# Optimization experiments

Measured on AMD Instinct MI355X. Metric: run time of the kernel, lower is better.

## Reference

```python
import jax, jax.numpy as jnp
import numpy as np

N = 50000          # nodes
E = 800000         # directed edges (before self-loops)
IN_C = 512
HID = 256
HEADS = 8
HEAD_C = HID // HEADS
OUT_C = 64
NEG_SLOPE = 0.2    # PyG GATConv default LeakyReLU slope
EPS = 1e-16        # PyG softmax denominator epsilon


def _gat_layer(h, src, dst, a_src, a_dst):
    """One GATConv propagate step (eval mode, no attention dropout).
    h: [N, H, C] transformed node features; src/dst: [Etot] edge endpoints.
    Returns aggregated [N, H, C]."""
    # per-node attention logits: [N, H]
    alpha_src = jnp.einsum('nhc,hc->nh', h, a_src)
    alpha_dst = jnp.einsum('nhc,hc->nh', h, a_dst)
    e = alpha_src[src] + alpha_dst[dst]                      # [Etot, H]
    e = jnp.where(e > 0, e, NEG_SLOPE * e)                   # LeakyReLU
    # segment softmax over incoming edges of each dst node
    e_max = jax.ops.segment_max(e, dst, num_segments=N)      # [N, H]
    e_exp = jnp.exp(e - e_max[dst])                          # [Etot, H]
    denom = jax.ops.segment_sum(e_exp, dst, num_segments=N)  # [N, H]
    alpha = e_exp / (denom[dst] + EPS)                       # [Etot, H]
    msg = alpha[:, :, None] * h[src]                         # [Etot, H, C]
    return jax.ops.segment_sum(msg, dst, num_segments=N)     # [N, H, C]


def setup_inputs() -> dict:
    key = jax.random.key(0)
    ks = jax.random.split(key, 10)
    s1 = 1.0 / np.sqrt(IN_C)
    s2 = 1.0 / np.sqrt(HID)
    return {
        'x': jax.random.normal(ks[0], (N, IN_C), jnp.float32),
        'edge_index': jax.random.randint(ks[1], (2, E), 0, N, dtype=jnp.int64),
        'W1': jax.random.normal(ks[2], (IN_C, HID), jnp.float32) * s1,
        'a_src1': jax.random.normal(ks[3], (HEADS, HEAD_C), jnp.float32) * 0.1,
        'a_dst1': jax.random.normal(ks[4], (HEADS, HEAD_C), jnp.float32) * 0.1,
        'b1': jnp.zeros((HID,), jnp.float32),
        'W2': jax.random.normal(ks[5], (HID, OUT_C), jnp.float32) * s2,
        'a_src2': jax.random.normal(ks[6], (1, OUT_C), jnp.float32) * 0.1,
        'a_dst2': jax.random.normal(ks[7], (1, OUT_C), jnp.float32) * 0.1,
        'b2': jnp.zeros((OUT_C,), jnp.float32),
    }


def reference(x, edge_index, W1, a_src1, a_dst1, b1, W2, a_src2, a_dst2, b2):
    # PyG GATConv: add self-loops (default add_self_loops=True)
    loops = jnp.arange(N, dtype=edge_index.dtype)
    src = jnp.concatenate([edge_index[0], loops])
    dst = jnp.concatenate([edge_index[1], loops])

    # conv1: heads=8, concat=True
    h1 = (x @ W1).reshape(N, HEADS, HEAD_C)
    h1 = _gat_layer(h1, src, dst, a_src1, a_dst1).reshape(N, HID) + b1
    h1 = jax.nn.elu(h1)

    # conv2: heads=1, concat=False (mean over 1 head == identity)
    h2 = (h1 @ W2).reshape(N, 1, OUT_C)
    out = _gat_layer(h2, src, dst, a_src2, a_dst2).mean(axis=1) + b2
    return out
```

## Files before the change

kernel.cpp:

```cpp
#include <hip/hip_runtime.h>

#define N_NODES 50000
#define M_PAD   50048
#define NBLK    196
#define E_EDGES 800000
#define E_TOT   (E_EDGES + N_NODES)
#define IN_C 512
#define HID 256
#define HEADS 8
#define OUT_C 64

typedef unsigned int uint;
typedef unsigned short ushort_t;
typedef __bf16 bf16x8 __attribute__((ext_vector_type(8)));
typedef float f32x4 __attribute__((ext_vector_type(4)));
typedef float f32x2 __attribute__((ext_vector_type(2)));

__device__ __forceinline__ float lrelu(float x) { return x > 0.f ? x : 0.2f * x; }

__device__ __forceinline__ unsigned short f2bf(float f) {
  uint u = __float_as_uint(f);
  u += 0x7FFF + ((u >> 16) & 1);
  return (unsigned short)(u >> 16);
}
__device__ __forceinline__ float bflo(uint u) { return __uint_as_float(u << 16); }
__device__ __forceinline__ float bfhi(uint u) { return __uint_as_float(u & 0xFFFF0000u); }
__device__ __forceinline__ f32x2 unp2(uint u) {
  f32x2 r; r.x = bflo(u); r.y = bfhi(u); return r;
}

__global__ void k_count(const int* __restrict__ ei, int* __restrict__ counts) {
  int e = blockIdx.x * blockDim.x + threadIdx.x;
  if (e >= E_TOT) return;
  int d = (e < E_EDGES) ? ei[E_EDGES + e] : (e - E_EDGES);
  atomicAdd(&counts[d], 1);
}

__global__ void k_bsum(const int* __restrict__ counts, int* __restrict__ bsum) {
  int i = blockIdx.x * 256 + threadIdx.x;
  int v = (i < N_NODES) ? counts[i] : 0;
  __shared__ int ws[4];
  int lane = threadIdx.x & 63, wid = threadIdx.x >> 6;
  #pragma unroll
  for (int off = 32; off; off >>= 1) v += __shfl_xor(v, off);
  if (lane == 0) ws[wid] = v;
  __syncthreads();
  if (threadIdx.x == 0) bsum[blockIdx.x] = ws[0] + ws[1] + ws[2] + ws[3];
}

__global__ void k_bscan(const int* __restrict__ bsum, int* __restrict__ boff) {
  int tid = threadIdx.x;
  int v = (tid < NBLK) ? bsum[tid] : 0;
  int lane = tid & 63, wid = tid >> 6;
  int x = v;
  #pragma unroll
  for (int off = 1; off < 64; off <<= 1) {
    int t = __shfl_up(x, off);
    if (lane >= off) x += t;
  }
  __shared__ int ws[4];
  if (lane == 63) ws[wid] = x;
  __syncthreads();
  int woff = 0;
  for (int w = 0; w < wid; w++) woff += ws[w];
  if (tid < NBLK) boff[tid] = x + woff - v;
}

__global__ void k_local(const int* __restrict__ counts, const int* __restrict__ boff,
                        int* __restrict__ indptr, int* __restrict__ wptr) {
  int b = blockIdx.x;
  int i = b * 256 + threadIdx.x;
  int v = (i < N_NODES) ? counts[i] : 0;
  int lane = threadIdx.x & 63, wid = threadIdx.x >> 6;
  int x = v;
  #pragma unroll
  for (int off = 1; off < 64; off <<= 1) {
    int t = __shfl_up(x, off);
    if (lane >= off) x += t;
  }
  __shared__ int ws[4];
  if (lane == 63) ws[wid] = x;
  __syncthreads();
  int woff = boff[b];
  for (int w = 0; w < wid; w++) woff += ws[w];
  int excl = woff + x - v;
  if (i < N_NODES) { indptr[i] = excl; wptr[i] = excl; }
  if (b == 0 && threadIdx.x == 0) indptr[N_NODES] = E_TOT;
}

__global__ void k_scatter(const int* __restrict__ ei, int* __restrict__ wptr,
                          int* __restrict__ csr_src) {
  int e = blockIdx.x * blockDim.x + threadIdx.x;
  if (e >= E_TOT) return;
  int s, d;
  if (e < E_EDGES) { s = ei[e]; d = ei[E_EDGES + e]; }
  else { s = d = e - E_EDGES; }
  int pos = atomicAdd(&wptr[d], 1);
  csr_src[pos] = s;
}

__global__ void k_conv_w1(const float* __restrict__ W1, ushort_t* __restrict__ w1t) {
  int t = blockIdx.x * blockDim.x + threadIdx.x;
  if (t >= HID * IN_C) return;
  int n = t >> 9, k = t & 511;
  w1t[t] = f2bf(W1[(size_t)k * HID + n]);
}
__global__ void k_conv_w2(const float* __restrict__ W2, ushort_t* __restrict__ w2t) {
  int t = blockIdx.x * blockDim.x + threadIdx.x;
  if (t >= OUT_C * HID) return;
  int n = t >> 8, k = t & 255;
  w2t[t] = f2bf(W2[(size_t)k * OUT_C + n]);
}

__global__ __launch_bounds__(512) void k_mm1(const float* __restrict__ A,
                                             const ushort_t* __restrict__ Bt,
                                             ushort_t* __restrict__ Cb) {
  __shared__ ushort_t sA[128][40];
  __shared__ ushort_t sB[256][40];
  int tid = threadIdx.x;
  int wid = tid >> 6, lane = tid & 63;
  int wm = wid >> 2, wn = wid & 3;
  int lr = lane & 15, kg = lane >> 4;
  int row0 = blockIdx.x * 128;
  f32x4 acc[4][4] = {};

  for (int k0 = 0; k0 < IN_C; k0 += 32) {
    {
      int r = tid >> 2, cs = (tid & 3) * 8;
      int gr = row0 + r;
      unsigned short v[8];
      if (gr < N_NODES) {
        const float* src = A + (size_t)gr * IN_C + k0 + cs;
        float4 f0 = *reinterpret_cast<const float4*>(src);
        float4 f1 = *reinterpret_cast<const float4*>(src + 4);
        v[0] = f2bf(f0.x); v[1] = f2bf(f0.y); v[2] = f2bf(f0.z); v[3] = f2bf(f0.w);
        v[4] = f2bf(f1.x); v[5] = f2bf(f1.y); v[6] = f2bf(f1.z); v[7] = f2bf(f1.w);
      } else {
        #pragma unroll
        for (int i = 0; i < 8; i++) v[i] = 0;
      }
      uint4 pk;
      pk.x = v[0] | ((uint)v[1] << 16); pk.y = v[2] | ((uint)v[3] << 16);
      pk.z = v[4] | ((uint)v[5] << 16); pk.w = v[6] | ((uint)v[7] << 16);
      *reinterpret_cast<uint4*>(&sA[r][cs]) = pk;
    }
    {
      int n = tid >> 1, ks = (tid & 1) * 16;
      const ushort_t* src = Bt + (size_t)n * IN_C + k0 + ks;
      uint4 v0 = *reinterpret_cast<const uint4*>(src);
      uint4 v1 = *reinterpret_cast<const uint4*>(src + 8);
      *reinterpret_cast<uint4*>(&sB[n][ks]) = v0;
      *reinterpret_cast<uint4*>(&sB[n][ks + 8]) = v1;
    }
    __syncthreads();

    bf16x8 af[4], bfr[4];
    #pragma unroll
    for (int i = 0; i < 4; i++)
      af[i] = *reinterpret_cast<const bf16x8*>(&sA[wm * 64 + i * 16 + lr][kg * 8]);
    #pragma unroll
    for (int j = 0; j < 4; j++)
      bfr[j] = *reinterpret_cast<const bf16x8*>(&sB[wn * 64 + j * 16 + lr][kg * 8]);
    #pragma unroll
    for (int i = 0; i < 4; i++)
      #pragma unroll
      for (int j = 0; j < 4; j++)
        acc[i][j] = __builtin_amdgcn_mfma_f32_16x16x32_bf16(af[i], bfr[j], acc[i][j], 0, 0, 0);
    __syncthreads();
  }

  #pragma unroll
  for (int i = 0; i < 4; i++) {
    #pragma unroll
    for (int j = 0; j < 4; j++) {
      int gc = wn * 64 + j * 16 + lr;
      #pragma unroll
      for (int q = 0; q < 4; q++) {
        int gr = row0 + wm * 64 + i * 16 + kg * 4 + q;
        if (gr < N_NODES) Cb[(size_t)gr * HID + gc] = f2bf(acc[i][j][q]);
      }
    }
  }
}

__global__ __launch_bounds__(256) void k_mm2(const ushort_t* __restrict__ At,
                                             const ushort_t* __restrict__ Bt,
                                             float* __restrict__ C) {
  __shared__ ushort_t sA[128][40];
  __shared__ ushort_t sB[64][40];
  int tid = threadIdx.x;
  int wid = tid >> 6, lane = tid & 63;
  int lr = lane & 15, kg = lane >> 4;
  int row0 = blockIdx.x * 128;
  f32x4 acc[2][4] = {};

  for (int kt = 0; kt < HID / 32; ++kt) {
    {
      const ushort_t* src = At + ((size_t)blockIdx.x * 8 + kt) * 4096 + tid * 16;
      uint4 v0 = *reinterpret_cast<const uint4*>(src);
      uint4 v1 = *reinterpret_cast<const uint4*>(src + 8);
      int r = tid >> 1, ks = (tid & 1) * 16;
      *reinterpret_cast<uint4*>(&sA[r][ks]) = v0;
      *reinterpret_cast<uint4*>(&sA[r][ks + 8]) = v1;
    }
    if (tid < 128) {
      int n = tid >> 1, ks = (tid & 1) * 16;
      const ushort_t* src = Bt + (size_t)n * HID + kt * 32 + ks;
      uint4 v0 = *reinterpret_cast<const uint4*>(src);
      uint4 v1 = *reinterpret_cast<const uint4*>(src + 8);
      *reinterpret_cast<uint4*>(&sB[n][ks]) = v0;
      *reinterpret_cast<uint4*>(&sB[n][ks + 8]) = v1;
    }
    __syncthreads();

    bf16x8 af[2], bfr[4];
    #pragma unroll
    for (int i = 0; i < 2; i++)
      af[i] = *reinterpret_cast<const bf16x8*>(&sA[wid * 32 + i * 16 + lr][kg * 8]);
    #pragma unroll
    for (int j = 0; j < 4; j++)
      bfr[j] = *reinterpret_cast<const bf16x8*>(&sB[j * 16 + lr][kg * 8]);
    #pragma unroll
    for (int i = 0; i < 2; i++)
      #pragma unroll
      for (int j = 0; j < 4; j++)
        acc[i][j] = __builtin_amdgcn_mfma_f32_16x16x32_bf16(af[i], bfr[j], acc[i][j], 0, 0, 0);
    __syncthreads();
  }

  #pragma unroll
  for (int i = 0; i < 2; i++) {
    #pragma unroll
    for (int j = 0; j < 4; j++) {
      int gc = j * 16 + lr;
      #pragma unroll
      for (int q = 0; q < 4; q++) {
        int gr = row0 + wid * 32 + i * 16 + kg * 4 + q;
        if (gr < N_NODES) C[(size_t)gr * OUT_C + gc] = acc[i][j][q];
      }
    }
  }
}

__global__ void k_alpha1(const ushort_t* __restrict__ h1b, const float* __restrict__ a_src,
                         const float* __restrict__ a_dst, float* __restrict__ as1,
                         float* __restrict__ ad1) {
  int t = blockIdx.x * blockDim.x + threadIdx.x;
  if (t >= N_NODES * HEADS) return;
  int n = t >> 3, h = t & 7;
  const ushort_t* row = h1b + (size_t)n * HID + h * 32;
  const float* asr = a_src + h * 32;
  const float* adr = a_dst + h * 32;
  float ss = 0.f, sd = 0.f;
  #pragma unroll
  for (int c = 0; c < 32; c += 8) {
    uint4 rv = *reinterpret_cast<const uint4*>(row + c);
    uint uu[4] = {rv.x, rv.y, rv.z, rv.w};
    #pragma unroll
    for (int q = 0; q < 4; q++) {
      float f0 = bflo(uu[q]), f1 = bfhi(uu[q]);
      ss += f0 * asr[c + q * 2] + f1 * asr[c + q * 2 + 1];
      sd += f0 * adr[c + q * 2] + f1 * adr[c + q * 2 + 1];
    }
  }
  as1[t] = ss;
  ad1[t] = sd;
}

__global__ void k_alpha2(const float* __restrict__ h2, const float* __restrict__ a_src,
                         const float* __restrict__ a_dst, float* __restrict__ as2,
                         float* __restrict__ ad2) {
  int wave = threadIdx.x >> 6, lane = threadIdx.x & 63;
  int n = blockIdx.x * 4 + wave;
  if (n >= N_NODES) return;
  float v = h2[(size_t)n * OUT_C + lane];
  float ss = v * a_src[lane];
  float sd = v * a_dst[lane];
  #pragma unroll
  for (int off = 32; off; off >>= 1) {
    ss += __shfl_xor(ss, off);
    sd += __shfl_xor(sd, off);
  }
  if (lane == 0) { as2[n] = ss; ad2[n] = sd; }
}

__global__ __launch_bounds__(256) void k_agg1(const ushort_t* __restrict__ h1b,
                                              const int* __restrict__ indptr,
                                              const int* __restrict__ csr_src,
                                              const float* __restrict__ as1,
                                              const float* __restrict__ ad1,
                                              const float* __restrict__ b1,
                                              ushort_t* __restrict__ hpb) {
  int wave = threadIdx.x >> 6, lane = threadIdx.x & 63;
  int node = blockIdx.x * 4 + wave;
  if (node >= N_NODES) return;
  int beg = indptr[node], end = indptr[node + 1];
  int half = lane >> 5, sl = lane & 31, h = sl >> 2;
  float adst = ad1[node * 8 + h];

  f32x2 a0 = {0.f, 0.f}, a1 = {0.f, 0.f}, a2 = {0.f, 0.f}, a3 = {0.f, 0.f};
  float dsum = 0.f;
  int e = beg + half;
  for (; e + 6 < end; e += 8) {
    int s0 = csr_src[e];
    int s1 = csr_src[e + 2];
    int s2 = csr_src[e + 4];
    int s3 = csr_src[e + 6];
    float l0 = as1[s0 * 8 + h];
    float l1 = as1[s1 * 8 + h];
    float l2 = as1[s2 * 8 + h];
    float l3 = as1[s3 * 8 + h];
    uint4 r0 = *reinterpret_cast<const uint4*>(&h1b[(size_t)s0 * HID + sl * 8]);
    uint4 r1 = *reinterpret_cast<const uint4*>(&h1b[(size_t)s1 * HID + sl * 8]);
    uint4 r2 = *reinterpret_cast<const uint4*>(&h1b[(size_t)s2 * HID + sl * 8]);
    uint4 r3 = *reinterpret_cast<const uint4*>(&h1b[(size_t)s3 * HID + sl * 8]);
    float w0 = __expf(lrelu(l0 + adst));
    float w1 = __expf(lrelu(l1 + adst));
    float w2 = __expf(lrelu(l2 + adst));
    float w3 = __expf(lrelu(l3 + adst));
    a0 += w0 * unp2(r0.x); a1 += w0 * unp2(r0.y); a2 += w0 * unp2(r0.z); a3 += w0 * unp2(r0.w);
    a0 += w1 * unp2(r1.x); a1 += w1 * unp2(r1.y); a2 += w1 * unp2(r1.z); a3 += w1 * unp2(r1.w);
    a0 += w2 * unp2(r2.x); a1 += w2 * unp2(r2.y); a2 += w2 * unp2(r2.z); a3 += w2 * unp2(r2.w);
    a0 += w3 * unp2(r3.x); a1 += w3 * unp2(r3.y); a2 += w3 * unp2(r3.z); a3 += w3 * unp2(r3.w);
    dsum += w0 + w1 + w2 + w3;
  }
  for (; e < end; e += 2) {
    int s = csr_src[e];
    float w = __expf(lrelu(as1[s * 8 + h] + adst));
    uint4 rv = *reinterpret_cast<const uint4*>(&h1b[(size_t)s * HID + sl * 8]);
    a0 += w * unp2(rv.x); a1 += w * unp2(rv.y); a2 += w * unp2(rv.z); a3 += w * unp2(rv.w);
    dsum += w;
  }
  float acc[8] = {a0.x, a0.y, a1.x, a1.y, a2.x, a2.y, a3.x, a3.y};
  #pragma unroll
  for (int j = 0; j < 8; j++) acc[j] += __shfl_xor(acc[j], 32);
  dsum += __shfl_xor(dsum, 32);
  float inv = 1.f / (dsum + 1e-16f);

  if (half == 0) {
    unsigned short ob[8];
    #pragma unroll
    for (int j = 0; j < 8; j++) {
      float o = acc[j] * inv + b1[sl * 8 + j];
      o = o > 0.f ? o : expm1f(o);
      ob[j] = f2bf(o);
    }
    uint4 pk;
    pk.x = ob[0] | ((uint)ob[1] << 16); pk.y = ob[2] | ((uint)ob[3] << 16);
    pk.z = ob[4] | ((uint)ob[5] << 16); pk.w = ob[6] | ((uint)ob[7] << 16);
    size_t addr = ((size_t)(node >> 7) * 8 + (sl >> 2)) * 4096 + (size_t)(node & 127) * 32 + (sl & 3) * 8;
    *reinterpret_cast<uint4*>(&hpb[addr]) = pk;
  }
}

__global__ __launch_bounds__(256) void k_agg2(const float* __restrict__ h2,
                                              const int* __restrict__ indptr,
                                              const int* __restrict__ csr_src,
                                              const float* __restrict__ as2,
                                              const float* __restrict__ ad2,
                                              const float* __restrict__ b2,
                                              float* __restrict__ out) {
  int wave = threadIdx.x >> 6, lane = threadIdx.x & 63;
  int node = blockIdx.x * 4 + wave;
  if (node >= N_NODES) return;
  int beg = indptr[node], end = indptr[node + 1];
  int half = lane >> 5, sl = lane & 31;
  float adst = ad2[node];

  f32x2 acc2 = {0.f, 0.f};
  float dsum = 0.f;
  int e = beg + half;
  for (; e + 6 < end; e += 8) {
    int s0 = csr_src[e];
    int s1 = csr_src[e + 2];
    int s2 = csr_src[e + 4];
    int s3 = csr_src[e + 6];
    float l0 = as2[s0];
    float l1 = as2[s1];
    float l2 = as2[s2];
    float l3 = as2[s3];
    f32x2 v0 = *reinterpret_cast<const f32x2*>(&h2[(size_t)s0 * OUT_C + sl * 2]);
    f32x2 v1 = *reinterpret_cast<const f32x2*>(&h2[(size_t)s1 * OUT_C + sl * 2]);
    f32x2 v2 = *reinterpret_cast<const f32x2*>(&h2[(size_t)s2 * OUT_C + sl * 2]);
    f32x2 v3 = *reinterpret_cast<const f32x2*>(&h2[(size_t)s3 * OUT_C + sl * 2]);
    float w0 = __expf(lrelu(l0 + adst));
    float w1 = __expf(lrelu(l1 + adst));
    float w2 = __expf(lrelu(l2 + adst));
    float w3 = __expf(lrelu(l3 + adst));
    acc2 += w0 * v0; acc2 += w1 * v1; acc2 += w2 * v2; acc2 += w3 * v3;
    dsum += w0 + w1 + w2 + w3;
  }
  for (; e < end; e += 2) {
    int s = csr_src[e];
    float w = __expf(lrelu(as2[s] + adst));
    f32x2 v = *reinterpret_cast<const f32x2*>(&h2[(size_t)s * OUT_C + sl * 2]);
    acc2 += w * v;
    dsum += w;
  }
  acc2.x += __shfl_xor(acc2.x, 32);
  acc2.y += __shfl_xor(acc2.y, 32);
  dsum += __shfl_xor(dsum, 32);
  float inv = 1.f / (dsum + 1e-16f);
  if (half == 0) {
    float2 o = {acc2.x * inv + b2[sl * 2], acc2.y * inv + b2[sl * 2 + 1]};
    *reinterpret_cast<float2*>(&out[(size_t)node * OUT_C + sl * 2]) = o;
  }
}

extern "C" void kernel_launch(void* const* d_in, const int* in_sizes, int n_in,
                              void* d_out, int out_size, void* d_ws, size_t ws_size,
                              hipStream_t stream) {
  const float* x     = (const float*)d_in[0];
  const int*   ei    = (const int*)d_in[1];
  const float* W1    = (const float*)d_in[2];
  const float* asrc1 = (const float*)d_in[3];
  const float* adst1 = (const float*)d_in[4];
  const float* b1    = (const float*)d_in[5];
  const float* W2    = (const float*)d_in[6];
  const float* asrc2 = (const float*)d_in[7];
  const float* adst2 = (const float*)d_in[8];
  const float* b2    = (const float*)d_in[9];
  float* out = (float*)d_out;

  char* p = (char*)d_ws;
  size_t off = 0;
  auto take = [&](size_t bytes) -> void* {
    void* r = p + off;
    off += (bytes + 255) & ~(size_t)255;
    return r;
  };
  ushort_t* h1b  = (ushort_t*)take((size_t)N_NODES * HID * 2);
  ushort_t* hpb  = (ushort_t*)take((size_t)(M_PAD / 128) * 8 * 4096 * 2);
  float*    h2   = (float*)take((size_t)N_NODES * OUT_C * 4);
  float*    as1  = (float*)take((size_t)N_NODES * HEADS * 4);
  float*    ad1  = (float*)take((size_t)N_NODES * HEADS * 4);
  float*    as2  = (float*)take((size_t)N_NODES * 4);
  float*    ad2  = (float*)take((size_t)N_NODES * 4);
  int* counts = (int*)take((size_t)N_NODES * 4);
  int* indptr = (int*)take((size_t)(N_NODES + 1) * 4);
  int* wptr   = (int*)take((size_t)(N_NODES + 1) * 4);
  int* bsum   = (int*)take((size_t)NBLK * 4);
  int* boff   = (int*)take((size_t)NBLK * 4);
  int* csr    = (int*)take((size_t)E_TOT * 4);
  ushort_t* w1t = (ushort_t*)take((size_t)IN_C * HID * 2);
  ushort_t* w2t = (ushort_t*)take((size_t)HID * OUT_C * 2);

  hipMemsetAsync(counts, 0, (size_t)N_NODES * 4, stream);
  k_count<<<(E_TOT + 255) / 256, 256, 0, stream>>>(ei, counts);
  k_bsum<<<NBLK, 256, 0, stream>>>(counts, bsum);
  k_bscan<<<1, 256, 0, stream>>>(bsum, boff);
  k_local<<<NBLK, 256, 0, stream>>>(counts, boff, indptr, wptr);
  k_scatter<<<(E_TOT + 255) / 256, 256, 0, stream>>>(ei, wptr, csr);

  k_conv_w1<<<(HID * IN_C + 255) / 256, 256, 0, stream>>>(W1, w1t);
  k_conv_w2<<<(OUT_C * HID + 255) / 256, 256, 0, stream>>>(W2, w2t);

  k_mm1<<<M_PAD / 128, 512, 0, stream>>>(x, w1t, h1b);
  k_alpha1<<<(N_NODES * HEADS + 255) / 256, 256, 0, stream>>>(h1b, asrc1, adst1, as1, ad1);
  k_agg1<<<(N_NODES + 3) / 4, 256, 0, stream>>>(h1b, indptr, csr, as1, ad1, b1, hpb);

  k_mm2<<<M_PAD / 128, 256, 0, stream>>>(hpb, w2t, h2);
  k_alpha2<<<(N_NODES + 3) / 4, 256, 0, stream>>>(h2, asrc2, adst2, as2, ad2);
  k_agg2<<<(N_NODES + 3) / 4, 256, 0, stream>>>(h2, indptr, csr, as2, ad2, b2, out);
}
```

Before: 286.3 us.

## Split layer-1 aggregation by head slot and store h2 as bf16

The layer-1 aggregation now launches 8 blocks per group of 4 nodes, each covering one head's 32 channels. Sixteen edge slots per wave each gather a 64-byte slice, and attention logits are stored head-major so each block reads one contiguous per-head array. The goal is to shrink the per-block working set and improve cache locality of the logit gathers, at the cost of reloading the indices 8 times and doing more shuffle reductions. Separately, the layer-2 features h2 are stored as bf16 instead of fp32, halving the gather traffic in the alpha2 and agg2 kernels at some precision cost.

```diff
diff --git a/kernel.cpp b/kernel.cpp
--- a/kernel.cpp
+++ b/kernel.cpp
@@ -25,6 +25,7 @@
 }
 __device__ __forceinline__ float bflo(uint u) { return __uint_as_float(u << 16); }
 __device__ __forceinline__ float bfhi(uint u) { return __uint_as_float(u & 0xFFFF0000u); }
+__device__ __forceinline__ float bf2f(ushort_t u) { return __uint_as_float(((uint)u) << 16); }
 __device__ __forceinline__ f32x2 unp2(uint u) {
   f32x2 r; r.x = bflo(u); r.y = bfhi(u); return r;
 }
@@ -185,7 +186,7 @@
 
 __global__ __launch_bounds__(256) void k_mm2(const ushort_t* __restrict__ At,
                                              const ushort_t* __restrict__ Bt,
-                                             float* __restrict__ C) {
+                                             ushort_t* __restrict__ Cb) {
   __shared__ ushort_t sA[128][40];
   __shared__ ushort_t sB[64][40];
   int tid = threadIdx.x;
@@ -236,15 +237,15 @@
       #pragma unroll
       for (int q = 0; q < 4; q++) {
         int gr = row0 + wid * 32 + i * 16 + kg * 4 + q;
-        if (gr < N_NODES) C[(size_t)gr * OUT_C + gc] = acc[i][j][q];
+        if (gr < N_NODES) Cb[(size_t)gr * OUT_C + gc] = f2bf(acc[i][j][q]);
       }
     }
   }
 }
 
 __global__ void k_alpha1(const ushort_t* __restrict__ h1b, const float* __restrict__ a_src,
-                         const float* __restrict__ a_dst, float* __restrict__ as1,
-                         float* __restrict__ ad1) {
+                         const float* __restrict__ a_dst, float* __restrict__ as1p,
+                         float* __restrict__ ad1p) {
   int t = blockIdx.x * blockDim.x + threadIdx.x;
   if (t >= N_NODES * HEADS) return;
   int n = t >> 3, h = t & 7;
@@ -263,17 +264,17 @@
       sd += f0 * adr[c + q * 2] + f1 * adr[c + q * 2 + 1];
     }
   }
-  as1[t] = ss;
-  ad1[t] = sd;
-}
-
-__global__ void k_alpha2(const float* __restrict__ h2, const float* __restrict__ a_src,
+  as1p[(size_t)h * N_NODES + n] = ss;
+  ad1p[(size_t)h * N_NODES + n] = sd;
+}
+
+__global__ void k_alpha2(const ushort_t* __restrict__ h2b, const float* __restrict__ a_src,
                          const float* __restrict__ a_dst, float* __restrict__ as2,
                          float* __restrict__ ad2) {
   int wave = threadIdx.x >> 6, lane = threadIdx.x & 63;
   int n = blockIdx.x * 4 + wave;
   if (n >= N_NODES) return;
-  float v = h2[(size_t)n * OUT_C + lane];
+  float v = bf2f(h2b[(size_t)n * OUT_C + lane]);
   float ss = v * a_src[lane];
   float sd = v * a_dst[lane];
   #pragma unroll
@@ -287,73 +288,71 @@
 __global__ __launch_bounds__(256) void k_agg1(const ushort_t* __restrict__ h1b,
                                               const int* __restrict__ indptr,
                                               const int* __restrict__ csr_src,
-                                              const float* __restrict__ as1,
-                                              const float* __restrict__ ad1,
+                                              const float* __restrict__ as1p,
+                                              const float* __restrict__ ad1p,
                                               const float* __restrict__ b1,
                                               ushort_t* __restrict__ hpb) {
+  int slot = blockIdx.x & 7;
   int wave = threadIdx.x >> 6, lane = threadIdx.x & 63;
-  int node = blockIdx.x * 4 + wave;
-  if (node >= N_NODES) return;
+  int node = (blockIdx.x >> 3) * 4 + wave;
   int beg = indptr[node], end = indptr[node + 1];
-  int half = lane >> 5, sl = lane & 31, h = sl >> 2;
-  float adst = ad1[node * 8 + h];
+  int eslot = lane >> 2, cl = lane & 3;
+  float adst = ad1p[(size_t)slot * N_NODES + node];
+  const float* asl = as1p + (size_t)slot * N_NODES;
+  const ushort_t* hq = h1b + slot * 32 + cl * 8;
 
   f32x2 a0 = {0.f, 0.f}, a1 = {0.f, 0.f}, a2 = {0.f, 0.f}, a3 = {0.f, 0.f};
   float dsum = 0.f;
-  int e = beg + half;
-  for (; e + 6 < end; e += 8) {
-    int s0 = csr_src[e];
-    int s1 = csr_src[e + 2];
-    int s2 = csr_src[e + 4];
-    int s3 = csr_src[e + 6];
-    float l0 = as1[s0 * 8 + h];
-    float l1 = as1[s1 * 8 + h];
-    float l2 = as1[s2 * 8 + h];
-    float l3 = as1[s3 * 8 + h];
-    uint4 r0 = *reinterpret_cast<const uint4*>(&h1b[(size_t)s0 * HID + sl * 8]);
-    uint4 r1 = *reinterpret_cast<const uint4*>(&h1b[(size_t)s1 * HID + sl * 8]);
-    uint4 r2 = *reinterpret_cast<const uint4*>(&h1b[(size_t)s2 * HID + sl * 8]);
-    uint4 r3 = *reinterpret_cast<const uint4*>(&h1b[(size_t)s3 * HID + sl * 8]);
+  int e = beg + eslot;
+  for (; e + 16 < end; e += 32) {
+    int s0 = __builtin_nontemporal_load(&csr_src[e]);
+    int s1 = __builtin_nontemporal_load(&csr_src[e + 16]);
+    float l0 = asl[s0];
+    float l1 = asl[s1];
+    uint4 r0 = *reinterpret_cast<const uint4*>(&hq[(size_t)s0 * HID]);
+    uint4 r1 = *reinterpret_cast<const uint4*>(&hq[(size_t)s1 * HID]);
     float w0 = __expf(lrelu(l0 + adst));
     float w1 = __expf(lrelu(l1 + adst));
-    float w2 = __expf(lrelu(l2 + adst));
-    float w3 = __expf(lrelu(l3 + adst));
     a0 += w0 * unp2(r0.x); a1 += w0 * unp2(r0.y); a2 += w0 * unp2(r0.z); a3 += w0 * unp2(r0.w);
     a0 += w1 * unp2(r1.x); a1 += w1 * unp2(r1.y); a2 += w1 * unp2(r1.z); a3 += w1 * unp2(r1.w);
-    a0 += w2 * unp2(r2.x); a1 += w2 * unp2(r2.y); a2 += w2 * unp2(r2.z); a3 += w2 * unp2(r2.w);
-    a0 += w3 * unp2(r3.x); a1 += w3 * unp2(r3.y); a2 += w3 * unp2(r3.z); a3 += w3 * unp2(r3.w);
-    dsum += w0 + w1 + w2 + w3;
-  }
-  for (; e < end; e += 2) {
-    int s = csr_src[e];
-    float w = __expf(lrelu(as1[s * 8 + h] + adst));
-    uint4 rv = *reinterpret_cast<const uint4*>(&h1b[(size_t)s * HID + sl * 8]);
+    dsum += w0 + w1;
+  }
+  for (; e < end; e += 16) {
+    int s = __builtin_nontemporal_load(&csr_src[e]);
+    float w = __expf(lrelu(asl[s] + adst));
+    uint4 rv = *reinterpret_cast<const uint4*>(&hq[(size_t)s * HID]);
     a0 += w * unp2(rv.x); a1 += w * unp2(rv.y); a2 += w * unp2(rv.z); a3 += w * unp2(rv.w);
     dsum += w;
   }
-  float acc[8] = {a0.x, a0.y, a1.x, a1.y, a2.x, a2.y, a3.x, a3.y};
-  #pragma unroll
-  for (int j = 0; j < 8; j++) acc[j] += __shfl_xor(acc[j], 32);
-  dsum += __shfl_xor(dsum, 32);
+  #pragma unroll
+  for (int off = 4; off <= 32; off <<= 1) {
+    a0.x += __shfl_xor(a0.x, off); a0.y += __shfl_xor(a0.y, off);
+    a1.x += __shfl_xor(a1.x, off); a1.y += __shfl_xor(a1.y, off);
+    a2.x += __shfl_xor(a2.x, off); a2.y += __shfl_xor(a2.y, off);
+    a3.x += __shfl_xor(a3.x, off); a3.y += __shfl_xor(a3.y, off);
+    dsum += __shfl_xor(dsum, off);
+  }
   float inv = 1.f / (dsum + 1e-16f);
 
-  if (half == 0) {
+  if (eslot == 0) {
+    float acc[8] = {a0.x, a0.y, a1.x, a1.y, a2.x, a2.y, a3.x, a3.y};
+    int c0 = slot * 32 + cl * 8;
     unsigned short ob[8];
     #pragma unroll
     for (int j = 0; j < 8; j++) {
-      float o = acc[j] * inv + b1[sl * 8 + j];
+      float o = acc[j] * inv + b1[c0 + j];
       o = o > 0.f ? o : expm1f(o);
       ob[j] = f2bf(o);
     }
     uint4 pk;
     pk.x = ob[0] | ((uint)ob[1] << 16); pk.y = ob[2] | ((uint)ob[3] << 16);
     pk.z = ob[4] | ((uint)ob[5] << 16); pk.w = ob[6] | ((uint)ob[7] << 16);
-    size_t addr = ((size_t)(node >> 7) * 8 + (sl >> 2)) * 4096 + (size_t)(node & 127) * 32 + (sl & 3) * 8;
+    size_t addr = ((size_t)(node >> 7) * 8 + slot) * 4096 + (size_t)(node & 127) * 32 + cl * 8;
     *reinterpret_cast<uint4*>(&hpb[addr]) = pk;
   }
 }
 
-__global__ __launch_bounds__(256) void k_agg2(const float* __restrict__ h2,
+__global__ __launch_bounds__(256) void k_agg2(const ushort_t* __restrict__ h2b,
                                               const int* __restrict__ indptr,
                                               const int* __restrict__ csr_src,
                                               const float* __restrict__ as2,
@@ -379,22 +378,23 @@
     float l1 = as2[s1];
     float l2 = as2[s2];
     float l3 = as2[s3];
-    f32x2 v0 = *reinterpret_cast<const f32x2*>(&h2[(size_t)s0 * OUT_C + sl * 2]);
-    f32x2 v1 = *reinterpret_cast<const f32x2*>(&h2[(size_t)s1 * OUT_C + sl * 2]);
-    f32x2 v2 = *reinterpret_cast<const f32x2*>(&h2[(size_t)s2 * OUT_C + sl * 2]);
-    f32x2 v3 = *reinterpret_cast<const f32x2*>(&h2[(size_t)s3 * OUT_C + sl * 2]);
+    uint v0 = *reinterpret_cast<const uint*>(&h2b[(size_t)s0 * OUT_C + sl * 2]);
+    uint v1 = *reinterpret_cast<const uint*>(&h2b[(size_t)s1 * OUT_C + sl * 2]);
+    uint v2 = *reinterpret_cast<const uint*>(&h2b[(size_t)s2 * OUT_C + sl * 2]);
+    uint v3 = *reinterpret_cast<const uint*>(&h2b[(size_t)s3 * OUT_C + sl * 2]);
     float w0 = __expf(lrelu(l0 + adst));
     float w1 = __expf(lrelu(l1 + adst));
     float w2 = __expf(lrelu(l2 + adst));
     float w3 = __expf(lrelu(l3 + adst));
-    acc2 += w0 * v0; acc2 += w1 * v1; acc2 += w2 * v2; acc2 += w3 * v3;
+    acc2 += w0 * unp2(v0); acc2 += w1 * unp2(v1);
+    acc2 += w2 * unp2(v2); acc2 += w3 * unp2(v3);
     dsum += w0 + w1 + w2 + w3;
   }
   for (; e < end; e += 2) {
     int s = csr_src[e];
     float w = __expf(lrelu(as2[s] + adst));
-    f32x2 v = *reinterpret_cast<const f32x2*>(&h2[(size_t)s * OUT_C + sl * 2]);
-    acc2 += w * v;
+    uint v = *reinterpret_cast<const uint*>(&h2b[(size_t)s * OUT_C + sl * 2]);
+    acc2 += w * unp2(v);
     dsum += w;
   }
   acc2.x += __shfl_xor(acc2.x, 32);
@@ -431,9 +431,9 @@
   };
   ushort_t* h1b  = (ushort_t*)take((size_t)N_NODES * HID * 2);
   ushort_t* hpb  = (ushort_t*)take((size_t)(M_PAD / 128) * 8 * 4096 * 2);
-  float*    h2   = (float*)take((size_t)N_NODES * OUT_C * 4);
-  float*    as1  = (float*)take((size_t)N_NODES * HEADS * 4);
-  float*    ad1  = (float*)take((size_t)N_NODES * HEADS * 4);
+  ushort_t* h2b  = (ushort_t*)take((size_t)N_NODES * OUT_C * 2);
+  float*    as1p = (float*)take((size_t)N_NODES * HEADS * 4);
+  float*    ad1p = (float*)take((size_t)N_NODES * HEADS * 4);
   float*    as2  = (float*)take((size_t)N_NODES * 4);
   float*    ad2  = (float*)take((size_t)N_NODES * 4);
   int* counts = (int*)take((size_t)N_NODES * 4);
@@ -456,10 +456,10 @@
   k_conv_w2<<<(OUT_C * HID + 255) / 256, 256, 0, stream>>>(W2, w2t);
 
   k_mm1<<<M_PAD / 128, 512, 0, stream>>>(x, w1t, h1b);
-  k_alpha1<<<(N_NODES * HEADS + 255) / 256, 256, 0, stream>>>(h1b, asrc1, adst1, as1, ad1);
-  k_agg1<<<(N_NODES + 3) / 4, 256, 0, stream>>>(h1b, indptr, csr, as1, ad1, b1, hpb);
-
-  k_mm2<<<M_PAD / 128, 256, 0, stream>>>(hpb, w2t, h2);
-  k_alpha2<<<(N_NODES + 3) / 4, 256, 0, stream>>>(h2, asrc2, adst2, as2, ad2);
-  k_agg2<<<(N_NODES + 3) / 4, 256, 0, stream>>>(h2, indptr, csr, as2, ad2, b2, out);
-}
+  k_alpha1<<<(N_NODES * HEADS + 255) / 256, 256, 0, stream>>>(h1b, asrc1, adst1, as1p, ad1p);
+  k_agg1<<<(N_NODES / 4) * 8, 256, 0, stream>>>(h1b, indptr, csr, as1p, ad1p, b1, hpb);
+
+  k_mm2<<<M_PAD / 128, 256, 0, stream>>>(hpb, w2t, h2b);
+  k_alpha2<<<(N_NODES + 3) / 4, 256, 0, stream>>>(h2b, asrc2, adst2, as2, ad2);
+  k_agg2<<<(N_NODES + 3) / 4, 256, 0, stream>>>(h2b, indptr, csr, as2, ad2, b2, out);
+}
```

New measurement: 499.3 us. 74.4% more time.
